# Kernel optimization log

Hardware: AMD Instinct MI355X
Metric: run time of the kernel (lower is better)

Reference implementation:

```python
import jax, jax.numpy as jnp
import numpy as np

N = 10000       # nodes
F_IN = 512      # input_features
E_DIM = 256     # embedding_features
H0, H1 = 512, 256  # fc layer widths (layers=[512,256]); fc input = 2*E_DIM = 512
N_EDGES = 160000


def setup_inputs() -> dict:
    key = jax.random.key(0)
    ks = jax.random.split(key, 10)
    feature = jax.random.normal(ks[0], (N, F_IN), jnp.float32)
    edge_src = jax.random.randint(ks[1], (N_EDGES,), 0, N, jnp.int32)
    edge_dst = jax.random.randint(ks[2], (N_EDGES,), 0, N, jnp.int32)
    def lin(k, fan_in, fan_out):
        return jax.random.normal(k, (fan_in, fan_out), jnp.float32) / np.sqrt(fan_in).astype(np.float32)
    We = lin(ks[3], F_IN, E_DIM);     be = jnp.zeros((E_DIM,), jnp.float32)
    W0 = lin(ks[4], 2 * E_DIM, H0);   b0 = jnp.zeros((H0,), jnp.float32)
    W1 = lin(ks[5], H0, H1);          b1 = jnp.zeros((H1,), jnp.float32)
    Wlk = lin(ks[6], H1, 1);          blk = jnp.zeros((1,), jnp.float32)
    Wa = lin(ks[7], H1, 2);           ba = jnp.zeros((2,), jnp.float32)
    return dict(feature=feature, We=We, be=be, W0=W0, b0=b0, W1=W1, b1=b1,
                Wlk=Wlk, blk=blk, Wa=Wa, ba=ba,
                edge_src=edge_src, edge_dst=edge_dst)


def reference(feature, We, be, W0, b0, W1, b1, Wlk, blk, Wa, ba, edge_src, edge_dst):
    # get_embedding: Linear + relu
    emb = jax.nn.relu(feature @ We + be)                      # [N, E]
    # Each node i has its neighbor entries plus one 'ending' entry paired with zeros
    seg = jnp.concatenate([edge_src, jnp.arange(N, dtype=edge_src.dtype)])     # [T]
    dst_all = jnp.concatenate([edge_dst, jnp.full((N,), -1, edge_dst.dtype)])  # -1 = ending sentinel
    nbr = jnp.concatenate([emb[edge_dst], jnp.zeros((N, E_DIM), emb.dtype)], axis=0)
    s = jnp.concatenate([emb[seg], nbr], axis=-1)             # [T, 2E]
    # fc MLP, then lk head
    h = jax.nn.relu(jax.nn.relu(s @ W0 + b0) @ W1 + b1)       # [T, H1]
    lk = (h @ Wlk + blk)[:, 0]                                # [T]
    # Deterministic greedy pick per node (argmax of lk == argmax of softmax(lk))
    best = jax.ops.segment_max(lk, seg, num_segments=N)       # [N]
    T = lk.shape[0]
    cand = jnp.where(lk == best[seg], jnp.arange(T, dtype=jnp.int32), -1)
    win = jax.ops.segment_max(cand, seg, num_segments=N)      # winning entry index per node
    chosen = dst_all[win]                                     # chosen neighbor (-1 = ending)
    # action head on the winning pair feature; argmax(softmax(logits)) == argmax(logits)
    logits = h[win] @ Wa + ba                                 # [N, 2]
    at = jnp.argmax(logits, axis=-1)
    do_upd = (chosen >= 0) & (at == 1)
    safe = jnp.clip(chosen, 0, N - 1)
    # hv = mean(feature_origin[i], feature_origin[chosen]) then re-embed
    mean_feat = 0.5 * (feature + feature[safe])               # [N, F]
    new_val = jax.nn.relu(mean_feat @ We + be)                # [N, E]
    tgt = jnp.where(do_upd, safe, N)                          # N = out of range -> dropped
    return emb.at[tgt].set(new_val, mode='drop')
```

## Files before the change

kernel.cpp:

```cpp
#include <hip/hip_runtime.h>
#include <stdint.h>

#define N_NODES 10000
#define F_IN    512
#define E_DIM   256
#define H0D     512
#define H1D     256
#define N_EDGES 160000
#define T_TOT   (N_EDGES + N_NODES)

#define MT 64
#define KB 32
#define MARGIN_LK 4e-3f
#define MARGIN_L  4e-3f
#define LIST_CAP 20000
#define FIX_GRID 1024
#define LP 40

typedef _Float16 f16;
typedef __attribute__((ext_vector_type(8))) _Float16 f16x8;
typedef __attribute__((ext_vector_type(4))) float f32x4;

__device__ __forceinline__ unsigned int f2ord(float f) {
    unsigned int u = __float_as_uint(f);
    return (u & 0x80000000u) ? ~u : (u | 0x80000000u);
}
__device__ __forceinline__ float ord2f(unsigned int o) {
    unsigned int u = (o & 0x80000000u) ? (o & 0x7fffffffu) : ~o;
    return __uint_as_float(u);
}

__global__ void k_prep_all(const float* __restrict__ We,
                           const float* __restrict__ W1,
                           const float* __restrict__ W0,
                           f16* __restrict__ WeC_h, f16* __restrict__ WeC_l,
                           f16* __restrict__ W1C_h, f16* __restrict__ W1C_l,
                           f16* __restrict__ W0C_h, f16* __restrict__ W0C_l,
                           float* __restrict__ W1T) {
    int b = blockIdx.x;
    int n = threadIdx.x;
    if (b >= 64) {
        int j = (b - 64) * 8 + (n >> 5);
        int k0 = (n & 31) * 16;
#pragma unroll
        for (int kk = 0; kk < 16; kk++)
            W1T[(size_t)j * 512 + k0 + kk] = W1[(size_t)(k0 + kk) * H1D + j];
        return;
    }
    const float* W;
    int ld, rowoff, colbase, c;
    f16 *dh_base, *dl_base;
    if (b < 16) {
        W = We; ld = E_DIM; rowoff = 0; colbase = 0; c = b;
        dh_base = WeC_h; dl_base = WeC_l;
    } else if (b < 32) {
        W = W1; ld = H1D; rowoff = 0; colbase = 0; c = b - 16;
        dh_base = W1C_h; dl_base = W1C_l;
    } else {
        int g = (b - 32) >> 3; c = (b - 32) & 7;
        rowoff = (g >= 2) ? 256 : 0; colbase = (g & 1) * 256;
        W = W0; ld = H0D;
        dh_base = W0C_h + (size_t)g * 8 * 256 * 32;
        dl_base = W0C_l + (size_t)g * 8 * 256 * 32;
    }
    f16* dh = dh_base + ((size_t)c * 256 + n) * 32;
    f16* dl = dl_base + ((size_t)c * 256 + n) * 32;
    const float* src = W + (size_t)(rowoff + c * 32) * ld + colbase + n;
#pragma unroll
    for (int kk = 0; kk < 32; kk++) {
        float w = src[(size_t)kk * ld];
        f16 h = (f16)w;
        f16 l = (f16)(w - (float)h);
        dh[kk] = h;
        dl[kk] = l;
    }
}

__global__ __launch_bounds__(256, 3) void k1_split(
        const float* __restrict__ feat, const f16* __restrict__ Bh_g,
        const f16* __restrict__ Bl_g, const float* __restrict__ be,
        float* __restrict__ Z, float* __restrict__ out) {
    __shared__ f16 Ah[64 * LP], Al_[64 * LP];
    __shared__ f16 Bh[256 * LP], Bl[256 * LP];
    const int tid = threadIdx.x;
    const int wave = tid >> 6, lane = tid & 63;
    const int quad = lane >> 4, l15 = lane & 15;
    const int mbase = blockIdx.x * 64;
    const int arow = tid >> 2, akp = tid & 3;
    const int gm_a = mbase + arow;
    const float* Arow = feat + (size_t)gm_a * F_IN + akp * 8;
    const bool rowok = (gm_a < N_NODES);

    f32x4 acc[4][4];
#pragma unroll
    for (int i = 0; i < 4; i++)
#pragma unroll
        for (int j = 0; j < 4; j++) acc[i][j] = (f32x4){0.f, 0.f, 0.f, 0.f};

    for (int k0 = 0; k0 < F_IN; k0 += 32) {
        float4 a0 = make_float4(0.f, 0.f, 0.f, 0.f), a1 = a0;
        if (rowok) {
            a0 = *(const float4*)(Arow + k0);
            a1 = *(const float4*)(Arow + k0 + 4);
        }
        f16x8 hv, lv;
        float av[8] = {a0.x, a0.y, a0.z, a0.w, a1.x, a1.y, a1.z, a1.w};
#pragma unroll
        for (int q = 0; q < 8; q++) {
            f16 h = (f16)av[q];
            hv[q] = h;
            lv[q] = (f16)(av[q] - (float)h);
        }
        const f16* bsh = Bh_g + (size_t)(k0 >> 5) * (256 * 32);
        const f16* bsl = Bl_g + (size_t)(k0 >> 5) * (256 * 32);
        f16x8 bvh[4], bvl[4];
#pragma unroll
        for (int r = 0; r < 4; r++) {
            bvh[r] = *(const f16x8*)(bsh + (size_t)(tid + 256 * r) * 8);
            bvl[r] = *(const f16x8*)(bsl + (size_t)(tid + 256 * r) * 8);
        }
        *(f16x8*)(Ah + arow * LP + akp * 8) = hv;
        *(f16x8*)(Al_ + arow * LP + akp * 8) = lv;
#pragma unroll
        for (int r = 0; r < 4; r++) {
            int f = tid + 256 * r;
            int n = f >> 2, kb = (f & 3) * 8;
            *(f16x8*)(Bh + n * LP + kb) = bvh[r];
            *(f16x8*)(Bl + n * LP + kb) = bvl[r];
        }
        __syncthreads();

        f16x8 afh[4], afl[4], bfh[4], bfl[4];
#pragma unroll
        for (int rt = 0; rt < 4; rt++) {
            afh[rt] = *(const f16x8*)(Ah + (rt * 16 + l15) * LP + quad * 8);
            afl[rt] = *(const f16x8*)(Al_ + (rt * 16 + l15) * LP + quad * 8);
        }
#pragma unroll
        for (int ct = 0; ct < 4; ct++) {
            bfh[ct] = *(const f16x8*)(Bh + (wave * 64 + ct * 16 + l15) * LP + quad * 8);
            bfl[ct] = *(const f16x8*)(Bl + (wave * 64 + ct * 16 + l15) * LP + quad * 8);
        }
#pragma unroll
        for (int rt = 0; rt < 4; rt++)
#pragma unroll
            for (int ct = 0; ct < 4; ct++) {
                acc[rt][ct] = __builtin_amdgcn_mfma_f32_16x16x32_f16(
                    afh[rt], bfh[ct], acc[rt][ct], 0, 0, 0);
                acc[rt][ct] = __builtin_amdgcn_mfma_f32_16x16x32_f16(
                    afl[rt], bfh[ct], acc[rt][ct], 0, 0, 0);
                acc[rt][ct] = __builtin_amdgcn_mfma_f32_16x16x32_f16(
                    afh[rt], bfl[ct], acc[rt][ct], 0, 0, 0);
            }
        __syncthreads();
    }

#pragma unroll
    for (int ct = 0; ct < 4; ct++) {
        int n = wave * 64 + ct * 16 + l15;
        float bb = be[n];
#pragma unroll
        for (int rt = 0; rt < 4; rt++)
#pragma unroll
            for (int reg = 0; reg < 4; reg++) {
                int gm = mbase + rt * 16 + quad * 4 + reg;
                if (gm < N_NODES) {
                    float z = acc[rt][ct][reg] + bb;
                    Z[(size_t)gm * E_DIM + n] = z;
                    out[(size_t)gm * E_DIM + n] = fmaxf(z, 0.f);
                }
            }
    }
}

__global__ __launch_bounds__(256, 3) void k2_split(
        const float* __restrict__ emb, const f16* __restrict__ W0Ch,
        const f16* __restrict__ W0Cl, const float* __restrict__ b0,
        float* __restrict__ P, float* __restrict__ Qm,
        f16* __restrict__ Pf, f16* __restrict__ Qf) {
    __shared__ f16 Ah[64 * LP], Al_[64 * LP];
    __shared__ f16 Bh[256 * LP], Bl[256 * LP];
    const int tid = threadIdx.x;
    const int wave = tid >> 6, lane = tid & 63;
    const int quad = lane >> 4, l15 = lane & 15;
    const int mbase = blockIdx.x * 64;
    const int g = blockIdx.y;
    const int isQ = (g >= 2);
    const int colbase = (g & 1) * 256;
    const int arow = tid >> 2, akp = tid & 3;
    const int gm_a = mbase + arow;
    const float* Arow = emb + (size_t)gm_a * E_DIM + akp * 8;
    const bool rowok = (gm_a < N_NODES);
    const f16* Bh_g = W0Ch + (size_t)g * 8 * 256 * 32;
    const f16* Bl_g = W0Cl + (size_t)g * 8 * 256 * 32;

    f32x4 acc[4][4];
#pragma unroll
    for (int i = 0; i < 4; i++)
#pragma unroll
        for (int j = 0; j < 4; j++) acc[i][j] = (f32x4){0.f, 0.f, 0.f, 0.f};

    for (int k0 = 0; k0 < E_DIM; k0 += 32) {
        float4 a0 = make_float4(0.f, 0.f, 0.f, 0.f), a1 = a0;
        if (rowok) {
            a0 = *(const float4*)(Arow + k0);
            a1 = *(const float4*)(Arow + k0 + 4);
        }
        f16x8 hv, lv;
        float av[8] = {a0.x, a0.y, a0.z, a0.w, a1.x, a1.y, a1.z, a1.w};
#pragma unroll
        for (int q = 0; q < 8; q++) {
            f16 h = (f16)av[q];
            hv[q] = h;
            lv[q] = (f16)(av[q] - (float)h);
        }
        const f16* bsh = Bh_g + (size_t)(k0 >> 5) * (256 * 32);
        const f16* bsl = Bl_g + (size_t)(k0 >> 5) * (256 * 32);
        f16x8 bvh[4], bvl[4];
#pragma unroll
        for (int r = 0; r < 4; r++) {
            bvh[r] = *(const f16x8*)(bsh + (size_t)(tid + 256 * r) * 8);
            bvl[r] = *(const f16x8*)(bsl + (size_t)(tid + 256 * r) * 8);
        }
        *(f16x8*)(Ah + arow * LP + akp * 8) = hv;
        *(f16x8*)(Al_ + arow * LP + akp * 8) = lv;
#pragma unroll
        for (int r = 0; r < 4; r++) {
            int f = tid + 256 * r;
            int n = f >> 2, kb = (f & 3) * 8;
            *(f16x8*)(Bh + n * LP + kb) = bvh[r];
            *(f16x8*)(Bl + n * LP + kb) = bvl[r];
        }
        __syncthreads();

        f16x8 afh[4], afl[4], bfh[4], bfl[4];
#pragma unroll
        for (int rt = 0; rt < 4; rt++) {
            afh[rt] = *(const f16x8*)(Ah + (rt * 16 + l15) * LP + quad * 8);
            afl[rt] = *(const f16x8*)(Al_ + (rt * 16 + l15) * LP + quad * 8);
        }
#pragma unroll
        for (int ct = 0; ct < 4; ct++) {
            bfh[ct] = *(const f16x8*)(Bh + (wave * 64 + ct * 16 + l15) * LP + quad * 8);
            bfl[ct] = *(const f16x8*)(Bl + (wave * 64 + ct * 16 + l15) * LP + quad * 8);
        }
#pragma unroll
        for (int rt = 0; rt < 4; rt++)
#pragma unroll
            for (int ct = 0; ct < 4; ct++) {
                acc[rt][ct] = __builtin_amdgcn_mfma_f32_16x16x32_f16(
                    afh[rt], bfh[ct], acc[rt][ct], 0, 0, 0);
                acc[rt][ct] = __builtin_amdgcn_mfma_f32_16x16x32_f16(
                    afl[rt], bfh[ct], acc[rt][ct], 0, 0, 0);
                acc[rt][ct] = __builtin_amdgcn_mfma_f32_16x16x32_f16(
                    afh[rt], bfl[ct], acc[rt][ct], 0, 0, 0);
            }
        __syncthreads();
    }

    float* dst = isQ ? Qm : P;
    f16* dstf = isQ ? Qf : Pf;
#pragma unroll
    for (int ct = 0; ct < 4; ct++) {
        int n = wave * 64 + ct * 16 + l15;
        float bb = isQ ? 0.f : b0[colbase + n];
#pragma unroll
        for (int rt = 0; rt < 4; rt++)
#pragma unroll
            for (int reg = 0; reg < 4; reg++) {
                int gm = mbase + rt * 16 + quad * 4 + reg;
                if (gm < N_NODES) {
                    float v = acc[rt][ct][reg] + bb;
                    dst[(size_t)gm * H0D + colbase + n] = v;
                    dstf[(size_t)gm * H0D + colbase + n] = (f16)v;
                }
            }
    }
}

__global__ __launch_bounds__(256, 3) void k3_f16(
        const f16* __restrict__ Pf, const f16* __restrict__ Qf,
        const f16* __restrict__ W1Bh, const float* __restrict__ b1,
        const float* __restrict__ Wlk, const float* __restrict__ blkp,
        const float* __restrict__ Wa, const float* __restrict__ ba,
        const int* __restrict__ esrc, const int* __restrict__ edst,
        unsigned long long* __restrict__ keys, float* __restrict__ lk_app,
        float* __restrict__ logits) {
    __shared__ f16 Ah[64 * LP];
    __shared__ f16 Bh[256 * LP];
    __shared__ float redA[64][5], redB[64][5], redC[64][5];
    __shared__ int s_seg[64], s_dst[64];
    const int tid = threadIdx.x;
    const int wave = tid >> 6, lane = tid & 63;
    const int quad = lane >> 4, l15 = lane & 15;
    const int tbase = blockIdx.x * 64;

    if (tid < 64) {
        int t = tbase + tid;
        int s = 0, d = -1;
        if (t < N_EDGES) { s = esrc[t]; d = edst[t]; }
        else if (t < T_TOT) { s = t - N_EDGES; }
        s_seg[tid] = s;
        s_dst[tid] = d;
    }
    __syncthreads();

    const int arow = tid >> 2, akp = tid & 3;
    const int sA = s_seg[arow], dA = s_dst[arow];
    const f16* Prow = Pf + (size_t)sA * H0D + akp * 8;
    const f16* Qrow = Qf + (size_t)(dA >= 0 ? dA : 0) * H0D + akp * 8;
    const bool hasQ = (dA >= 0);
    const f16x8 zero8 = (f16x8)(f16)0;

    f32x4 acc[4][4];
#pragma unroll
    for (int i = 0; i < 4; i++)
#pragma unroll
        for (int j = 0; j < 4; j++) acc[i][j] = (f32x4){0.f, 0.f, 0.f, 0.f};

    f16x8 pa = *(const f16x8*)(Prow);
    f16x8 qa = hasQ ? *(const f16x8*)(Qrow) : zero8;
    f16x8 bv[4];
#pragma unroll
    for (int r = 0; r < 4; r++)
        bv[r] = *(const f16x8*)(W1Bh + (size_t)(tid + 256 * r) * 8);

    for (int c = 0; c < 16; c++) {
        f16x8 hv;
#pragma unroll
        for (int q = 0; q < 8; q++) {
            f16 s = pa[q] + qa[q];
            hv[q] = (s > (f16)0) ? s : (f16)0;
        }
        *(f16x8*)(Ah + arow * LP + akp * 8) = hv;
#pragma unroll
        for (int r = 0; r < 4; r++) {
            int f = tid + 256 * r;
            int n = f >> 2, kb = (f & 3) * 8;
            *(f16x8*)(Bh + n * LP + kb) = bv[r];
        }
        __syncthreads();

        if (c + 1 < 16) {
            pa = *(const f16x8*)(Prow + (c + 1) * 32);
            qa = hasQ ? *(const f16x8*)(Qrow + (c + 1) * 32) : zero8;
            const f16* bsrc = W1Bh + (size_t)(c + 1) * (256 * 32);
#pragma unroll
            for (int r = 0; r < 4; r++)
                bv[r] = *(const f16x8*)(bsrc + (size_t)(tid + 256 * r) * 8);
        }

        f16x8 af[4], bf[4];
#pragma unroll
        for (int rt = 0; rt < 4; rt++)
            af[rt] = *(const f16x8*)(Ah + (rt * 16 + l15) * LP + quad * 8);
#pragma unroll
        for (int ct = 0; ct < 4; ct++)
            bf[ct] = *(const f16x8*)(Bh + (wave * 64 + ct * 16 + l15) * LP + quad * 8);
#pragma unroll
        for (int rt = 0; rt < 4; rt++)
#pragma unroll
            for (int ct = 0; ct < 4; ct++)
                acc[rt][ct] = __builtin_amdgcn_mfma_f32_16x16x32_f16(
                    af[rt], bf[ct], acc[rt][ct], 0, 0, 0);
        __syncthreads();
    }

    float wl[4], wa0[4], wa1[4], bb[4];
#pragma unroll
    for (int ct = 0; ct < 4; ct++) {
        int n = wave * 64 + ct * 16 + l15;
        wl[ct] = Wlk[n];
        wa0[ct] = Wa[2 * n];
        wa1[ct] = Wa[2 * n + 1];
        bb[ct] = b1[n];
    }
#pragma unroll
    for (int rt = 0; rt < 4; rt++) {
#pragma unroll
        for (int reg = 0; reg < 4; reg++) {
            float plk = 0.f, p0 = 0.f, p1 = 0.f;
#pragma unroll
            for (int ct = 0; ct < 4; ct++) {
                float h = fmaxf(acc[rt][ct][reg] + bb[ct], 0.f);
                plk = fmaf(h, wl[ct], plk);
                p0 = fmaf(h, wa0[ct], p0);
                p1 = fmaf(h, wa1[ct], p1);
            }
#pragma unroll
            for (int off = 8; off >= 1; off >>= 1) {
                plk += __shfl_xor(plk, off);
                p0 += __shfl_xor(p0, off);
                p1 += __shfl_xor(p1, off);
            }
            if (l15 == 0) {
                int row = rt * 16 + quad * 4 + reg;
                redA[row][wave] = plk;
                redB[row][wave] = p0;
                redC[row][wave] = p1;
            }
        }
    }
    __syncthreads();
    if (tid < 64) {
        int t = tbase + tid;
        if (t < T_TOT) {
            float lk = redA[tid][0] + redA[tid][1] + redA[tid][2] + redA[tid][3] + blkp[0];
            float l0 = redB[tid][0] + redB[tid][1] + redB[tid][2] + redB[tid][3] + ba[0];
            float l1 = redC[tid][0] + redC[tid][1] + redC[tid][2] + redC[tid][3] + ba[1];
            lk_app[t] = lk;
            logits[2 * t] = l0;
            logits[2 * t + 1] = l1;
            unsigned long long key =
                ((unsigned long long)f2ord(lk) << 32) | (unsigned int)t;
            atomicMax(keys + s_seg[tid], key);
        }
    }
}

__global__ void k_gb(const float* __restrict__ lk_app,
                     const unsigned long long* __restrict__ keys,
                     const int* __restrict__ esrc,
                     const float* __restrict__ logits,
                     int* __restrict__ list, int* __restrict__ count) {
    int t = blockIdx.x * 256 + threadIdx.x;
    if (t < T_TOT) {
        int seg = (t < N_EDGES) ? esrc[t] : t - N_EDGES;
        unsigned long long k = keys[seg];
        int tw = (int)(k & 0xFFFFFFFFull);
        if (t != tw) {
            float best = ord2f((unsigned int)(k >> 32));
            if (lk_app[t] >= best - MARGIN_LK) {
                int idx = atomicAdd(count, 2);
                if (idx + 1 < LIST_CAP) { list[idx] = t; list[idx + 1] = tw; }
            }
        }
    }
    if (t < N_NODES) {
        int tw = (int)(keys[t] & 0xFFFFFFFFull);
        float g = fabsf(logits[2 * tw + 1] - logits[2 * tw]);
        if (g < MARGIN_L) {
            int idx = atomicAdd(count, 1);
            if (idx < LIST_CAP) list[idx] = tw;
        }
    }
}

__global__ __launch_bounds__(256, 4) void k_fixup(
        const float* __restrict__ P, const float* __restrict__ Qm,
        const float* __restrict__ W1T, const float* __restrict__ b1,
        const float* __restrict__ Wlk, const float* __restrict__ blkp,
        const float* __restrict__ Wa, const float* __restrict__ ba,
        const int* __restrict__ esrc, const int* __restrict__ edst,
        const int* __restrict__ list, const int* __restrict__ count,
        unsigned long long* __restrict__ keys2, float* __restrict__ logits) {
    __shared__ float h1[512];
    __shared__ float red[3][4];
    const int tid = threadIdx.x;
    int cnt = *count;
    if (cnt > LIST_CAP) cnt = LIST_CAP;

    const float bb = b1[tid];
    const float wl = Wlk[tid];
    const float w0 = Wa[2 * tid];
    const float w1 = Wa[2 * tid + 1];
    const float* wrow = W1T + (size_t)tid * 512;

    for (int e = blockIdx.x; e < cnt; e += gridDim.x) {
        int t = list[e];
        if (t < 0 || t >= T_TOT) continue;
        int s, d;
        if (t < N_EDGES) { s = esrc[t]; d = edst[t]; }
        else { s = t - N_EDGES; d = -1; }

#pragma unroll
        for (int r = 0; r < 2; r++) {
            int k = tid + 256 * r;
            float v = P[(size_t)s * H0D + k];
            if (d >= 0) v += Qm[(size_t)d * H0D + k];
            h1[k] = fmaxf(v, 0.f);
        }
        __syncthreads();

        float a0 = 0.f, a1 = 0.f, a2 = 0.f, a3 = 0.f;
        for (int k = 0; k < 512; k += 16) {
            float4 wv0 = *(const float4*)(wrow + k);
            float4 wv1 = *(const float4*)(wrow + k + 4);
            float4 wv2 = *(const float4*)(wrow + k + 8);
            float4 wv3 = *(const float4*)(wrow + k + 12);
            float4 hv0 = *(const float4*)(h1 + k);
            float4 hv1 = *(const float4*)(h1 + k + 4);
            float4 hv2 = *(const float4*)(h1 + k + 8);
            float4 hv3 = *(const float4*)(h1 + k + 12);
            a0 = fmaf(hv0.x, wv0.x, a0); a0 = fmaf(hv0.y, wv0.y, a0);
            a0 = fmaf(hv0.z, wv0.z, a0); a0 = fmaf(hv0.w, wv0.w, a0);
            a1 = fmaf(hv1.x, wv1.x, a1); a1 = fmaf(hv1.y, wv1.y, a1);
            a1 = fmaf(hv1.z, wv1.z, a1); a1 = fmaf(hv1.w, wv1.w, a1);
            a2 = fmaf(hv2.x, wv2.x, a2); a2 = fmaf(hv2.y, wv2.y, a2);
            a2 = fmaf(hv2.z, wv2.z, a2); a2 = fmaf(hv2.w, wv2.w, a2);
            a3 = fmaf(hv3.x, wv3.x, a3); a3 = fmaf(hv3.y, wv3.y, a3);
            a3 = fmaf(hv3.z, wv3.z, a3); a3 = fmaf(hv3.w, wv3.w, a3);
        }
        float hj = fmaxf((a0 + a1) + (a2 + a3) + bb, 0.f);
        float plk = hj * wl;
        float p0 = hj * w0;
        float p1 = hj * w1;
#pragma unroll
        for (int off = 32; off >= 1; off >>= 1) {
            plk += __shfl_xor(plk, off);
            p0 += __shfl_xor(p0, off);
            p1 += __shfl_xor(p1, off);
        }
        int wv = tid >> 6;
        if ((tid & 63) == 0) {
            red[0][wv] = plk; red[1][wv] = p0; red[2][wv] = p1;
        }
        __syncthreads();
        if (tid == 0) {
            float lk = red[0][0] + red[0][1] + red[0][2] + red[0][3] + blkp[0];
            float l0 = red[1][0] + red[1][1] + red[1][2] + red[1][3] + ba[0];
            float l1 = red[2][0] + red[2][1] + red[2][2] + red[2][3] + ba[1];
            logits[2 * t] = l0;
            logits[2 * t + 1] = l1;
            unsigned long long key =
                ((unsigned long long)f2ord(lk) << 32) | (unsigned int)t;
            atomicMax(keys2 + s, key);
        }
        __syncthreads();
    }
}

__global__ void k4_select(const unsigned long long* __restrict__ keys,
                          const unsigned long long* __restrict__ keys2,
                          const int* __restrict__ edst,
                          const float* __restrict__ logits,
                          int* __restrict__ chosen_arr,
                          int* __restrict__ tgt_writer) {
    int i = blockIdx.x * 256 + threadIdx.x;
    if (i >= N_NODES) return;
    unsigned long long key = keys[i];
    unsigned long long k2v = keys2[i];
    if (k2v != 0ull) key = k2v;
    int t = (int)(key & 0xFFFFFFFFull);
    int chosen = (t < N_EDGES) ? edst[t] : -1;
    float lg0 = logits[2 * t], lg1 = logits[2 * t + 1];
    int at1 = (lg1 > lg0) ? 1 : 0;
    int c = (chosen >= 0 && at1) ? chosen : -1;
    chosen_arr[i] = c;
    if (c >= 0) atomicMax(tgt_writer + c, i + 1);
}

__global__ void k5_update(const int* __restrict__ chosen_arr,
                          const int* __restrict__ tgt_writer,
                          const float* __restrict__ Z,
                          float* __restrict__ out) {
    int i = blockIdx.x;
    int c = chosen_arr[i];
    if (c < 0 || tgt_writer[c] != i + 1) return;
    int n = threadIdx.x;
    float z = 0.5f * (Z[(size_t)i * E_DIM + n] + Z[(size_t)c * E_DIM + n]);
    out[(size_t)c * E_DIM + n] = fmaxf(z, 0.f);
}

extern "C" void kernel_launch(void* const* d_in, const int* in_sizes, int n_in,
                              void* d_out, int out_size, void* d_ws,
                              size_t ws_size, hipStream_t stream) {
    const float* feat = (const float*)d_in[0];
    const float* We   = (const float*)d_in[1];
    const float* be   = (const float*)d_in[2];
    const float* W0   = (const float*)d_in[3];
    const float* b0   = (const float*)d_in[4];
    const float* W1   = (const float*)d_in[5];
    const float* b1   = (const float*)d_in[6];
    const float* Wlk  = (const float*)d_in[7];
    const float* blkp = (const float*)d_in[8];
    const float* Wa   = (const float*)d_in[9];
    const float* ba   = (const float*)d_in[10];
    const int* esrc   = (const int*)d_in[11];
    const int* edst   = (const int*)d_in[12];
    float* out = (float*)d_out;

    char* ws = (char*)d_ws;
    size_t off = 0;
    float* Z  = (float*)(ws + off); off += (size_t)N_NODES * E_DIM * 4;
    float* P  = (float*)(ws + off); off += (size_t)N_NODES * H0D * 4;
    float* Qm = (float*)(ws + off); off += (size_t)N_NODES * H0D * 4;
    f16* Pf   = (f16*)(ws + off);   off += (size_t)N_NODES * H0D * 2;
    f16* Qf   = (f16*)(ws + off);   off += (size_t)N_NODES * H0D * 2;
    char* zero_base = ws + off;
    unsigned long long* keys  = (unsigned long long*)(ws + off); off += N_NODES * 8;
    unsigned long long* keys2 = (unsigned long long*)(ws + off); off += N_NODES * 8;
    int* tgt_writer = (int*)(ws + off); off += N_NODES * 4;
    int* count      = (int*)(ws + off); off += 128;
    size_t zero_bytes = (size_t)((ws + off) - zero_base);
    float* logits = (float*)(ws + off); off += (size_t)T_TOT * 2 * 4;
    float* lk_app = (float*)(ws + off); off += (size_t)T_TOT * 4;
    int* list     = (int*)(ws + off); off += (size_t)LIST_CAP * 4;
    int* chosen_arr = (int*)(ws + off); off += N_NODES * 4;
    f16* WeC_h = (f16*)(ws + off); off += (size_t)16 * 256 * 32 * 2;
    f16* WeC_l = (f16*)(ws + off); off += (size_t)16 * 256 * 32 * 2;
    f16* W1C_h = (f16*)(ws + off); off += (size_t)16 * 256 * 32 * 2;
    f16* W1C_l = (f16*)(ws + off); off += (size_t)16 * 256 * 32 * 2;
    f16* W0C_h = (f16*)(ws + off); off += (size_t)32 * 256 * 32 * 2;
    f16* W0C_l = (f16*)(ws + off); off += (size_t)32 * 256 * 32 * 2;
    float* W1T = (float*)(ws + off); off += (size_t)H1D * H0D * 4;

    hipMemsetAsync(zero_base, 0, zero_bytes, stream);

    k_prep_all<<<dim3(96), 256, 0, stream>>>(
        We, W1, W0, WeC_h, WeC_l, W1C_h, W1C_l, W0C_h, W0C_l, W1T);
    k1_split<<<dim3((N_NODES + 63) / 64), 256, 0, stream>>>(
        feat, WeC_h, WeC_l, be, Z, out);
    k2_split<<<dim3((N_NODES + 63) / 64, 4), 256, 0, stream>>>(
        out, W0C_h, W0C_l, b0, P, Qm, Pf, Qf);
    k3_f16<<<dim3((T_TOT + 63) / 64), 256, 0, stream>>>(
        Pf, Qf, W1C_h, b1, Wlk, blkp, Wa, ba, esrc, edst,
        keys, lk_app, logits);
    k_gb<<<dim3((T_TOT + 255) / 256), 256, 0, stream>>>(
        lk_app, keys, esrc, logits, list, count);
    k_fixup<<<dim3(FIX_GRID), 256, 0, stream>>>(
        P, Qm, W1T, b1, Wlk, blkp, Wa, ba, esrc, edst, list, count, keys2, logits);
    k4_select<<<dim3((N_NODES + 255) / 256), 256, 0, stream>>>(
        keys, keys2, edst, logits, chosen_arr, tgt_writer);
    k5_update<<<dim3(N_NODES), 256, 0, stream>>>(chosen_arr, tgt_writer, Z, out);
}
```

Baseline: 330.1 us.

## Load B fragments directly into registers and recompute fixup layer-0 from embeddings

The GEMM kernels (k1, k2, k3) no longer stage weight tiles through shared memory. Each wave now loads its B fragments straight from the pre-chunked global layout into registers, prefetched one K-chunk ahead. k1 moves to 32-row tiles, which doubles its grid. k2 no longer writes the fp32 P/Qm intermediates, and k_fixup instead recomputes the first fc layer in fp32 from the embeddings and W0 for each flagged entry. This removes LDS traffic and about 40 MB of fp32 writes. In exchange, the fixup pass does more work per entry, and every row tile reloads the same weights from global memory or cache.

```diff
diff --git a/kernel.cpp b/kernel.cpp
--- a/kernel.cpp
+++ b/kernel.cpp
@@ -9,8 +9,6 @@
 #define N_EDGES 160000
 #define T_TOT   (N_EDGES + N_NODES)
 
-#define MT 64
-#define KB 32
 #define MARGIN_LK 4e-3f
 #define MARGIN_L  4e-3f
 #define LIST_CAP 20000
@@ -19,6 +17,7 @@
 
 typedef _Float16 f16;
 typedef __attribute__((ext_vector_type(8))) _Float16 f16x8;
+typedef __attribute__((ext_vector_type(4))) _Float16 f16x4;
 typedef __attribute__((ext_vector_type(4))) float f32x4;
 
 __device__ __forceinline__ unsigned int f2ord(float f) {
@@ -76,83 +75,77 @@
     }
 }
 
-__global__ __launch_bounds__(256, 3) void k1_split(
+__global__ __launch_bounds__(256, 2) void k1_split(
         const float* __restrict__ feat, const f16* __restrict__ Bh_g,
         const f16* __restrict__ Bl_g, const float* __restrict__ be,
         float* __restrict__ Z, float* __restrict__ out) {
-    __shared__ f16 Ah[64 * LP], Al_[64 * LP];
-    __shared__ f16 Bh[256 * LP], Bl[256 * LP];
+    __shared__ f16 Ah[32 * LP], Al_[32 * LP];
     const int tid = threadIdx.x;
     const int wave = tid >> 6, lane = tid & 63;
     const int quad = lane >> 4, l15 = lane & 15;
-    const int mbase = blockIdx.x * 64;
-    const int arow = tid >> 2, akp = tid & 3;
+    const int mbase = blockIdx.x * 32;
+    const int arow = tid >> 3, apos = tid & 7;
     const int gm_a = mbase + arow;
-    const float* Arow = feat + (size_t)gm_a * F_IN + akp * 8;
+    const float* Arow = feat + (size_t)gm_a * F_IN + apos * 4;
     const bool rowok = (gm_a < N_NODES);
 
-    f32x4 acc[4][4];
-#pragma unroll
-    for (int i = 0; i < 4; i++)
+    f32x4 acc[2][4];
+#pragma unroll
+    for (int i = 0; i < 2; i++)
 #pragma unroll
         for (int j = 0; j < 4; j++) acc[i][j] = (f32x4){0.f, 0.f, 0.f, 0.f};
 
-    for (int k0 = 0; k0 < F_IN; k0 += 32) {
-        float4 a0 = make_float4(0.f, 0.f, 0.f, 0.f), a1 = a0;
-        if (rowok) {
-            a0 = *(const float4*)(Arow + k0);
-            a1 = *(const float4*)(Arow + k0 + 4);
-        }
-        f16x8 hv, lv;
-        float av[8] = {a0.x, a0.y, a0.z, a0.w, a1.x, a1.y, a1.z, a1.w};
-#pragma unroll
-        for (int q = 0; q < 8; q++) {
+    f16x8 bh[4], bl[4], bhn[4], bln[4];
+#pragma unroll
+    for (int ct = 0; ct < 4; ct++) {
+        size_t o = ((size_t)(wave * 64 + ct * 16 + l15)) * 32 + quad * 8;
+        bh[ct] = *(const f16x8*)(Bh_g + o);
+        bl[ct] = *(const f16x8*)(Bl_g + o);
+    }
+    float4 a = rowok ? *(const float4*)(Arow) : make_float4(0.f, 0.f, 0.f, 0.f);
+
+    for (int c = 0; c < 16; c++) {
+        f16x4 hv, lv;
+        float av[4] = {a.x, a.y, a.z, a.w};
+#pragma unroll
+        for (int q = 0; q < 4; q++) {
             f16 h = (f16)av[q];
             hv[q] = h;
             lv[q] = (f16)(av[q] - (float)h);
         }
-        const f16* bsh = Bh_g + (size_t)(k0 >> 5) * (256 * 32);
-        const f16* bsl = Bl_g + (size_t)(k0 >> 5) * (256 * 32);
-        f16x8 bvh[4], bvl[4];
-#pragma unroll
-        for (int r = 0; r < 4; r++) {
-            bvh[r] = *(const f16x8*)(bsh + (size_t)(tid + 256 * r) * 8);
-            bvl[r] = *(const f16x8*)(bsl + (size_t)(tid + 256 * r) * 8);
-        }
-        *(f16x8*)(Ah + arow * LP + akp * 8) = hv;
-        *(f16x8*)(Al_ + arow * LP + akp * 8) = lv;
-#pragma unroll
-        for (int r = 0; r < 4; r++) {
-            int f = tid + 256 * r;
-            int n = f >> 2, kb = (f & 3) * 8;
-            *(f16x8*)(Bh + n * LP + kb) = bvh[r];
-            *(f16x8*)(Bl + n * LP + kb) = bvl[r];
-        }
-        __syncthreads();
-
-        f16x8 afh[4], afl[4], bfh[4], bfl[4];
-#pragma unroll
-        for (int rt = 0; rt < 4; rt++) {
+        *(f16x4*)(Ah + arow * LP + apos * 4) = hv;
+        *(f16x4*)(Al_ + arow * LP + apos * 4) = lv;
+        if (c + 1 < 16) {
+            a = rowok ? *(const float4*)(Arow + (c + 1) * 32)
+                      : make_float4(0.f, 0.f, 0.f, 0.f);
+#pragma unroll
+            for (int ct = 0; ct < 4; ct++) {
+                size_t o = ((size_t)((c + 1) * 256 + wave * 64 + ct * 16 + l15)) * 32 + quad * 8;
+                bhn[ct] = *(const f16x8*)(Bh_g + o);
+                bln[ct] = *(const f16x8*)(Bl_g + o);
+            }
+        }
+        __syncthreads();
+        f16x8 afh[2], afl[2];
+#pragma unroll
+        for (int rt = 0; rt < 2; rt++) {
             afh[rt] = *(const f16x8*)(Ah + (rt * 16 + l15) * LP + quad * 8);
             afl[rt] = *(const f16x8*)(Al_ + (rt * 16 + l15) * LP + quad * 8);
         }
 #pragma unroll
-        for (int ct = 0; ct < 4; ct++) {
-            bfh[ct] = *(const f16x8*)(Bh + (wave * 64 + ct * 16 + l15) * LP + quad * 8);
-            bfl[ct] = *(const f16x8*)(Bl + (wave * 64 + ct * 16 + l15) * LP + quad * 8);
-        }
-#pragma unroll
-        for (int rt = 0; rt < 4; rt++)
+        for (int rt = 0; rt < 2; rt++)
 #pragma unroll
             for (int ct = 0; ct < 4; ct++) {
                 acc[rt][ct] = __builtin_amdgcn_mfma_f32_16x16x32_f16(
-                    afh[rt], bfh[ct], acc[rt][ct], 0, 0, 0);
+                    afh[rt], bh[ct], acc[rt][ct], 0, 0, 0);
                 acc[rt][ct] = __builtin_amdgcn_mfma_f32_16x16x32_f16(
-                    afl[rt], bfh[ct], acc[rt][ct], 0, 0, 0);
+                    afl[rt], bh[ct], acc[rt][ct], 0, 0, 0);
                 acc[rt][ct] = __builtin_amdgcn_mfma_f32_16x16x32_f16(
-                    afh[rt], bfl[ct], acc[rt][ct], 0, 0, 0);
-            }
-        __syncthreads();
+                    afh[rt], bl[ct], acc[rt][ct], 0, 0, 0);
+            }
+        __syncthreads();
+#pragma unroll
+        for (int ct = 0; ct < 4; ct++) { bh[ct] = bhn[ct]; bl[ct] = bln[ct]; }
     }
 
 #pragma unroll
@@ -160,7 +153,7 @@
         int n = wave * 64 + ct * 16 + l15;
         float bb = be[n];
 #pragma unroll
-        for (int rt = 0; rt < 4; rt++)
+        for (int rt = 0; rt < 2; rt++)
 #pragma unroll
             for (int reg = 0; reg < 4; reg++) {
                 int gm = mbase + rt * 16 + quad * 4 + reg;
@@ -176,10 +169,8 @@
 __global__ __launch_bounds__(256, 3) void k2_split(
         const float* __restrict__ emb, const f16* __restrict__ W0Ch,
         const f16* __restrict__ W0Cl, const float* __restrict__ b0,
-        float* __restrict__ P, float* __restrict__ Qm,
         f16* __restrict__ Pf, f16* __restrict__ Qf) {
     __shared__ f16 Ah[64 * LP], Al_[64 * LP];
-    __shared__ f16 Bh[256 * LP], Bl[256 * LP];
     const int tid = threadIdx.x;
     const int wave = tid >> 6, lane = tid & 63;
     const int quad = lane >> 4, l15 = lane & 15;
@@ -200,12 +191,17 @@
 #pragma unroll
         for (int j = 0; j < 4; j++) acc[i][j] = (f32x4){0.f, 0.f, 0.f, 0.f};
 
-    for (int k0 = 0; k0 < E_DIM; k0 += 32) {
-        float4 a0 = make_float4(0.f, 0.f, 0.f, 0.f), a1 = a0;
-        if (rowok) {
-            a0 = *(const float4*)(Arow + k0);
-            a1 = *(const float4*)(Arow + k0 + 4);
-        }
+    f16x8 bh[4], bl[4], bhn[4], bln[4];
+#pragma unroll
+    for (int ct = 0; ct < 4; ct++) {
+        size_t o = ((size_t)(wave * 64 + ct * 16 + l15)) * 32 + quad * 8;
+        bh[ct] = *(const f16x8*)(Bh_g + o);
+        bl[ct] = *(const f16x8*)(Bl_g + o);
+    }
+    float4 a0 = make_float4(0.f, 0.f, 0.f, 0.f), a1 = a0;
+    if (rowok) { a0 = *(const float4*)(Arow); a1 = *(const float4*)(Arow + 4); }
+
+    for (int c = 0; c < 8; c++) {
         f16x8 hv, lv;
         float av[8] = {a0.x, a0.y, a0.z, a0.w, a1.x, a1.y, a1.z, a1.w};
 #pragma unroll
@@ -214,51 +210,43 @@
             hv[q] = h;
             lv[q] = (f16)(av[q] - (float)h);
         }
-        const f16* bsh = Bh_g + (size_t)(k0 >> 5) * (256 * 32);
-        const f16* bsl = Bl_g + (size_t)(k0 >> 5) * (256 * 32);
-        f16x8 bvh[4], bvl[4];
-#pragma unroll
-        for (int r = 0; r < 4; r++) {
-            bvh[r] = *(const f16x8*)(bsh + (size_t)(tid + 256 * r) * 8);
-            bvl[r] = *(const f16x8*)(bsl + (size_t)(tid + 256 * r) * 8);
-        }
         *(f16x8*)(Ah + arow * LP + akp * 8) = hv;
         *(f16x8*)(Al_ + arow * LP + akp * 8) = lv;
-#pragma unroll
-        for (int r = 0; r < 4; r++) {
-            int f = tid + 256 * r;
-            int n = f >> 2, kb = (f & 3) * 8;
-            *(f16x8*)(Bh + n * LP + kb) = bvh[r];
-            *(f16x8*)(Bl + n * LP + kb) = bvl[r];
-        }
-        __syncthreads();
-
-        f16x8 afh[4], afl[4], bfh[4], bfl[4];
+        if (c + 1 < 8) {
+            if (rowok) {
+                a0 = *(const float4*)(Arow + (c + 1) * 32);
+                a1 = *(const float4*)(Arow + (c + 1) * 32 + 4);
+            }
+#pragma unroll
+            for (int ct = 0; ct < 4; ct++) {
+                size_t o = ((size_t)((c + 1) * 256 + wave * 64 + ct * 16 + l15)) * 32 + quad * 8;
+                bhn[ct] = *(const f16x8*)(Bh_g + o);
+                bln[ct] = *(const f16x8*)(Bl_g + o);
+            }
+        }
+        __syncthreads();
+        f16x8 afh[4], afl[4];
 #pragma unroll
         for (int rt = 0; rt < 4; rt++) {
             afh[rt] = *(const f16x8*)(Ah + (rt * 16 + l15) * LP + quad * 8);
             afl[rt] = *(const f16x8*)(Al_ + (rt * 16 + l15) * LP + quad * 8);
         }
 #pragma unroll
-        for (int ct = 0; ct < 4; ct++) {
-            bfh[ct] = *(const f16x8*)(Bh + (wave * 64 + ct * 16 + l15) * LP + quad * 8);
-            bfl[ct] = *(const f16x8*)(Bl + (wave * 64 + ct * 16 + l15) * LP + quad * 8);
-        }
-#pragma unroll
         for (int rt = 0; rt < 4; rt++)
 #pragma unroll
             for (int ct = 0; ct < 4; ct++) {
                 acc[rt][ct] = __builtin_amdgcn_mfma_f32_16x16x32_f16(
-                    afh[rt], bfh[ct], acc[rt][ct], 0, 0, 0);
+                    afh[rt], bh[ct], acc[rt][ct], 0, 0, 0);
                 acc[rt][ct] = __builtin_amdgcn_mfma_f32_16x16x32_f16(
-                    afl[rt], bfh[ct], acc[rt][ct], 0, 0, 0);
+                    afl[rt], bh[ct], acc[rt][ct], 0, 0, 0);
                 acc[rt][ct] = __builtin_amdgcn_mfma_f32_16x16x32_f16(
-                    afh[rt], bfl[ct], acc[rt][ct], 0, 0, 0);
-            }
-        __syncthreads();
-    }
-
-    float* dst = isQ ? Qm : P;
+                    afh[rt], bl[ct], acc[rt][ct], 0, 0, 0);
+            }
+        __syncthreads();
+#pragma unroll
+        for (int ct = 0; ct < 4; ct++) { bh[ct] = bhn[ct]; bl[ct] = bln[ct]; }
+    }
+
     f16* dstf = isQ ? Qf : Pf;
 #pragma unroll
     for (int ct = 0; ct < 4; ct++) {
@@ -269,11 +257,8 @@
 #pragma unroll
             for (int reg = 0; reg < 4; reg++) {
                 int gm = mbase + rt * 16 + quad * 4 + reg;
-                if (gm < N_NODES) {
-                    float v = acc[rt][ct][reg] + bb;
-                    dst[(size_t)gm * H0D + colbase + n] = v;
-                    dstf[(size_t)gm * H0D + colbase + n] = (f16)v;
-                }
+                if (gm < N_NODES)
+                    dstf[(size_t)gm * H0D + colbase + n] = (f16)(acc[rt][ct][reg] + bb);
             }
     }
 }
@@ -287,7 +272,6 @@
         unsigned long long* __restrict__ keys, float* __restrict__ lk_app,
         float* __restrict__ logits) {
     __shared__ f16 Ah[64 * LP];
-    __shared__ f16 Bh[256 * LP];
     __shared__ float redA[64][5], redB[64][5], redC[64][5];
     __shared__ int s_seg[64], s_dst[64];
     const int tid = threadIdx.x;
@@ -320,10 +304,10 @@
 
     f16x8 pa = *(const f16x8*)(Prow);
     f16x8 qa = hasQ ? *(const f16x8*)(Qrow) : zero8;
-    f16x8 bv[4];
-#pragma unroll
-    for (int r = 0; r < 4; r++)
-        bv[r] = *(const f16x8*)(W1Bh + (size_t)(tid + 256 * r) * 8);
+    f16x8 bf[4], bfn[4];
+#pragma unroll
+    for (int ct = 0; ct < 4; ct++)
+        bf[ct] = *(const f16x8*)(W1Bh + ((size_t)(wave * 64 + ct * 16 + l15)) * 32 + quad * 8);
 
     for (int c = 0; c < 16; c++) {
         f16x8 hv;
@@ -333,30 +317,19 @@
             hv[q] = (s > (f16)0) ? s : (f16)0;
         }
         *(f16x8*)(Ah + arow * LP + akp * 8) = hv;
-#pragma unroll
-        for (int r = 0; r < 4; r++) {
-            int f = tid + 256 * r;
-            int n = f >> 2, kb = (f & 3) * 8;
-            *(f16x8*)(Bh + n * LP + kb) = bv[r];
-        }
-        __syncthreads();
-
         if (c + 1 < 16) {
             pa = *(const f16x8*)(Prow + (c + 1) * 32);
             qa = hasQ ? *(const f16x8*)(Qrow + (c + 1) * 32) : zero8;
-            const f16* bsrc = W1Bh + (size_t)(c + 1) * (256 * 32);
-#pragma unroll
-            for (int r = 0; r < 4; r++)
-                bv[r] = *(const f16x8*)(bsrc + (size_t)(tid + 256 * r) * 8);
-        }
-
-        f16x8 af[4], bf[4];
+#pragma unroll
+            for (int ct = 0; ct < 4; ct++)
+                bfn[ct] = *(const f16x8*)(W1Bh +
+                    ((size_t)((c + 1) * 256 + wave * 64 + ct * 16 + l15)) * 32 + quad * 8);
+        }
+        __syncthreads();
+        f16x8 af[4];
 #pragma unroll
         for (int rt = 0; rt < 4; rt++)
             af[rt] = *(const f16x8*)(Ah + (rt * 16 + l15) * LP + quad * 8);
-#pragma unroll
-        for (int ct = 0; ct < 4; ct++)
-            bf[ct] = *(const f16x8*)(Bh + (wave * 64 + ct * 16 + l15) * LP + quad * 8);
 #pragma unroll
         for (int rt = 0; rt < 4; rt++)
 #pragma unroll
@@ -364,6 +337,8 @@
                 acc[rt][ct] = __builtin_amdgcn_mfma_f32_16x16x32_f16(
                     af[rt], bf[ct], acc[rt][ct], 0, 0, 0);
         __syncthreads();
+#pragma unroll
+        for (int ct = 0; ct < 4; ct++) bf[ct] = bfn[ct];
     }
 
     float wl[4], wa0[4], wa1[4], bb[4];
@@ -447,24 +422,28 @@
 }
 
 __global__ __launch_bounds__(256, 4) void k_fixup(
-        const float* __restrict__ P, const float* __restrict__ Qm,
-        const float* __restrict__ W1T, const float* __restrict__ b1,
-        const float* __restrict__ Wlk, const float* __restrict__ blkp,
-        const float* __restrict__ Wa, const float* __restrict__ ba,
-        const int* __restrict__ esrc, const int* __restrict__ edst,
-        const int* __restrict__ list, const int* __restrict__ count,
-        unsigned long long* __restrict__ keys2, float* __restrict__ logits) {
+        const float* __restrict__ emb, const float* __restrict__ W0,
+        const float* __restrict__ b0, const float* __restrict__ W1T,
+        const float* __restrict__ b1, const float* __restrict__ Wlk,
+        const float* __restrict__ blkp, const float* __restrict__ Wa,
+        const float* __restrict__ ba, const int* __restrict__ esrc,
+        const int* __restrict__ edst, const int* __restrict__ list,
+        const int* __restrict__ count, unsigned long long* __restrict__ keys2,
+        float* __restrict__ logits) {
+    __shared__ float embs[256], embd[256];
     __shared__ float h1[512];
     __shared__ float red[3][4];
     const int tid = threadIdx.x;
     int cnt = *count;
     if (cnt > LIST_CAP) cnt = LIST_CAP;
 
-    const float bb = b1[tid];
+    const float bb1 = b1[tid];
     const float wl = Wlk[tid];
-    const float w0 = Wa[2 * tid];
-    const float w1 = Wa[2 * tid + 1];
+    const float w0a = Wa[2 * tid];
+    const float w1a = Wa[2 * tid + 1];
     const float* wrow = W1T + (size_t)tid * 512;
+    const float bb0a = b0[tid];
+    const float bb0b = b0[tid + 256];
 
     for (int e = blockIdx.x; e < cnt; e += gridDim.x) {
         int t = list[e];
@@ -473,13 +452,21 @@
         if (t < N_EDGES) { s = esrc[t]; d = edst[t]; }
         else { s = t - N_EDGES; d = -1; }
 
-#pragma unroll
-        for (int r = 0; r < 2; r++) {
-            int k = tid + 256 * r;
-            float v = P[(size_t)s * H0D + k];
-            if (d >= 0) v += Qm[(size_t)d * H0D + k];
-            h1[k] = fmaxf(v, 0.f);
-        }
+        embs[tid] = emb[(size_t)s * E_DIM + tid];
+        embd[tid] = (d >= 0) ? emb[(size_t)d * E_DIM + tid] : 0.f;
+        __syncthreads();
+
+        float acc0 = bb0a, acc1 = bb0b;
+        for (int j = 0; j < 256; j++) {
+            float es = embs[j];
+            float ed = embd[j];
+            acc0 = fmaf(es, W0[(size_t)j * H0D + tid], acc0);
+            acc1 = fmaf(es, W0[(size_t)j * H0D + tid + 256], acc1);
+            acc0 = fmaf(ed, W0[(size_t)(256 + j) * H0D + tid], acc0);
+            acc1 = fmaf(ed, W0[(size_t)(256 + j) * H0D + tid + 256], acc1);
+        }
+        h1[tid] = fmaxf(acc0, 0.f);
+        h1[tid + 256] = fmaxf(acc1, 0.f);
         __syncthreads();
 
         float a0 = 0.f, a1 = 0.f, a2 = 0.f, a3 = 0.f;
@@ -501,10 +488,10 @@
             a3 = fmaf(hv3.x, wv3.x, a3); a3 = fmaf(hv3.y, wv3.y, a3);
             a3 = fmaf(hv3.z, wv3.z, a3); a3 = fmaf(hv3.w, wv3.w, a3);
         }
-        float hj = fmaxf((a0 + a1) + (a2 + a3) + bb, 0.f);
+        float hj = fmaxf((a0 + a1) + (a2 + a3) + bb1, 0.f);
         float plk = hj * wl;
-        float p0 = hj * w0;
-        float p1 = hj * w1;
+        float p0 = hj * w0a;
+        float p1 = hj * w1a;
 #pragma unroll
         for (int off = 32; off >= 1; off >>= 1) {
             plk += __shfl_xor(plk, off);
@@ -583,8 +570,6 @@
     char* ws = (char*)d_ws;
     size_t off = 0;
     float* Z  = (float*)(ws + off); off += (size_t)N_NODES * E_DIM * 4;
-    float* P  = (float*)(ws + off); off += (size_t)N_NODES * H0D * 4;
-    float* Qm = (float*)(ws + off); off += (size_t)N_NODES * H0D * 4;
     f16* Pf   = (f16*)(ws + off);   off += (size_t)N_NODES * H0D * 2;
     f16* Qf   = (f16*)(ws + off);   off += (size_t)N_NODES * H0D * 2;
     char* zero_base = ws + off;
@@ -609,17 +594,18 @@
 
     k_prep_all<<<dim3(96), 256, 0, stream>>>(
         We, W1, W0, WeC_h, WeC_l, W1C_h, W1C_l, W0C_h, W0C_l, W1T);
-    k1_split<<<dim3((N_NODES + 63) / 64), 256, 0, stream>>>(
+    k1_split<<<dim3((N_NODES + 31) / 32), 256, 0, stream>>>(
         feat, WeC_h, WeC_l, be, Z, out);
     k2_split<<<dim3((N_NODES + 63) / 64, 4), 256, 0, stream>>>(
-        out, W0C_h, W0C_l, b0, P, Qm, Pf, Qf);
+        out, W0C_h, W0C_l, b0, Pf, Qf);
     k3_f16<<<dim3((T_TOT + 63) / 64), 256, 0, stream>>>(
         Pf, Qf, W1C_h, b1, Wlk, blkp, Wa, ba, esrc, edst,
         keys, lk_app, logits);
     k_gb<<<dim3((T_TOT + 255) / 256), 256, 0, stream>>>(
         lk_app, keys, esrc, logits, list, count);
     k_fixup<<<dim3(FIX_GRID), 256, 0, stream>>>(
-        P, Qm, W1T, b1, Wlk, blkp, Wa, ba, esrc, edst, list, count, keys2, logits);
+        out, W0, b0, W1T, b1, Wlk, blkp, Wa, ba, esrc, edst,
+        list, count, keys2, logits);
     k4_select<<<dim3((N_NODES + 255) / 256), 256, 0, stream>>>(
         keys, keys2, edst, logits, chosen_arr, tgt_writer);
     k5_update<<<dim3(N_NODES), 256, 0, stream>>>(chosen_arr, tgt_writer, Z, out);
```

Result: no change. 336.1 us (+1.8%).
